# Optimization experiments

Measured on AMD Instinct MI355X. Metric: run time of the kernel, lower is better.

## Reference

```python
import jax, jax.numpy as jnp
import numpy as np

N, M, KNN, KUP, POS_DIM = 15872, 35637, 5, 20, 32


def _pos_emb_table(n, d):
    # transformer-style sinusoidal table (matches PosEmb._define_pos_emb)
    pos = np.arange(n, dtype=np.float32)[:, None]
    i2 = np.arange(0, d, 2, dtype=np.float32)
    div = 10000.0 ** (i2 / d)
    pe = np.zeros((n, d), dtype=np.float32)
    pe[:, 0::2] = np.sin(pos / div)
    pe[:, 1::2] = np.cos(pos / div)
    return jnp.asarray(pe)


def _lrelu(x):
    return jnp.where(x > 0, x, 0.2 * x)


def _gather(x, idx):
    # x: [B,n,d], idx: [B,m,k] -> [B,m,k,d]
    return jax.vmap(lambda xb, ib: xb[ib])(x, idx)


def _knn_idx(x, k):
    # x: [B,n,d]; k nearest excluding self (torch knn drops column 0 of topk)
    xx = jnp.sum(x * x, axis=-1)
    neg = 2.0 * jnp.einsum('bnd,bmd->bnm', x, x) - xx[:, :, None] - xx[:, None, :]
    _, idx = jax.lax.top_k(neg, k + 1)
    return idx[..., 1:]


def _emb_block(feat, idx, ec_w1, ec_s1, ec_h1, ec_w2, ec_b2,
               w1, s1, h1, w2, s2, h2, w3, s3, h3, w4, b4):
    # get_graph_feature: [B,n,k,2*in] = cat(nbr - ctr, ctr)
    nbr = _gather(feat, idx)
    ctr = jnp.broadcast_to(feat[:, :, None, :], nbr.shape)
    e = jnp.concatenate([nbr - ctr, ctr], axis=-1)
    # edge_conv (1x1 conv2d = per-edge linear); BN folded into scale/shift (eval mode)
    e = _lrelu(jnp.einsum('bnkc,oc->bnko', e, ec_w1) * ec_s1 + ec_h1)
    e = jnp.einsum('bnkc,oc->bnko', e, ec_w2) + ec_b2
    f1 = jnp.max(e, axis=2)                                   # max over k neighbors -> [B,n,out]
    fmax = jnp.broadcast_to(jnp.max(f1, axis=1, keepdims=True), f1.shape)
    favg = jnp.broadcast_to(jnp.mean(f1, axis=1, keepdims=True), f1.shape)
    h = jnp.concatenate([feat, f1, fmax, favg], axis=-1)      # [B,n,3*out+in]
    # fc_out: 1x1 conv1d stack = per-point MLP with folded BN + LeakyReLU
    h = _lrelu(h @ w1.T * s1 + h1)
    h = _lrelu(h @ w2.T * s2 + h2)
    h = _lrelu(h @ w3.T * s3 + h3)
    return h @ w4.T + b4


def _forward(lx, ldx, pos_emb,
             b0_ec_w1, b0_ec_s1, b0_ec_h1, b0_ec_w2, b0_ec_b2,
             b0_fc_w1, b0_fc_s1, b0_fc_h1, b0_fc_w2, b0_fc_s2, b0_fc_h2,
             b0_fc_w3, b0_fc_s3, b0_fc_h3, b0_fc_w4, b0_fc_b4,
             b1_ec_w1, b1_ec_s1, b1_ec_h1, b1_ec_w2, b1_ec_b2,
             b1_fc_w1, b1_fc_s1, b1_fc_h1, b1_fc_w2, b1_fc_s2, b1_fc_h2,
             b1_fc_w3, b1_fc_s3, b1_fc_h3, b1_fc_w4, b1_fc_b4,
             up_inputs, up_w0, up_s0, up_h0, up_w_rest, up_s_rest, up_h_rest, up_wf, up_bf,
             dec_w0, dec_b0, dec_w1, dec_b1, dec_w2, dec_b2, dec_w3, dec_b3,
             dec_w4, dec_b4, dec_wf, dec_bf,
             idx0, up_idx):
    B = ldx.shape[0]
    feat_in = jnp.concatenate([ldx, jnp.broadcast_to(pos_emb[None], (B,) + pos_emb.shape)], axis=-1)  # [B,N,35]
    f0 = _emb_block(feat_in, idx0,
                    b0_ec_w1, b0_ec_s1, b0_ec_h1, b0_ec_w2, b0_ec_b2,
                    b0_fc_w1, b0_fc_s1, b0_fc_h1, b0_fc_w2, b0_fc_s2, b0_fc_h2,
                    b0_fc_w3, b0_fc_s3, b0_fc_h3, b0_fc_w4, b0_fc_b4)   # [B,N,64]
    idx1 = _knn_idx(f0, KNN)                                            # dynamic feature-space KNN
    f1 = _emb_block(f0, idx1,
                    b1_ec_w1, b1_ec_s1, b1_ec_h1, b1_ec_w2, b1_ec_b2,
                    b1_fc_w1, b1_fc_s1, b1_fc_h1, b1_fc_w2, b1_fc_s2, b1_fc_h2,
                    b1_fc_w3, b1_fc_s3, b1_fc_h3, b1_fc_w4, b1_fc_b4)   # [B,N,128]
    x_feat = jnp.concatenate([feat_in, f0, f1], axis=-1)                # [B,N,227]
    # Upscale: SIREN-activated 1x1-conv stack -> softmax interpolation weights over KUP lo-res nbrs
    h = jnp.sin(jnp.einsum('bmkc,oc->bmko', up_inputs[:B], up_w0) * up_s0 + up_h0)
    for i in range(up_w_rest.shape[0]):
        h = jnp.sin(jnp.einsum('bmkc,oc->bmko', h, up_w_rest[i]) * up_s_rest[i] + up_h_rest[i])
    logits = jnp.einsum('bmkc,oc->bmko', h, up_wf) + up_bf              # [B,M,KUP,1]
    w = jax.nn.softmax(logits, axis=2)
    grouped = _gather(x_feat, up_idx)                                   # [B,M,KUP,227]
    z = jnp.sum(w * grouped, axis=2)                                    # [B,M,227]
    # SIREN decoder: dims [227,256,128,64,32,16,3]; zip with 5 mods applies first 5 layers + head
    h = jnp.sin(30.0 * (z @ dec_w0.T + dec_b0))
    h = jnp.sin(h @ dec_w1.T + dec_b1)
    h = jnp.sin(h @ dec_w2.T + dec_b2)
    h = jnp.sin(h @ dec_w3.T + dec_b3)
    h = jnp.sin(h @ dec_w4.T + dec_b4)
    return h @ dec_wf.T + dec_bf                                        # [B,M,3]


def setup_inputs():
    key = jax.random.key(0)
    ks = iter(jax.random.split(key, 100))
    def rn(*s):
        return jax.random.normal(next(ks), s, jnp.float32) * 0.05
    def sc(*s):
        return jax.random.uniform(next(ks), s, jnp.float32, minval=0.5, maxval=1.5)
    inp = {}
    inp['lx'] = jax.random.normal(next(ks), (1, N, 3), jnp.float32)
    inp['ldx'] = jax.random.normal(next(ks), (1, N, 3), jnp.float32)
    inp['pos_emb'] = _pos_emb_table(N, POS_DIM)
    inp['idx0'] = jax.random.randint(next(ks), (1, N, KNN), 0, N - 1)
    # EmbModule 0: in=35, out=64
    inp['b0_ec_w1'], inp['b0_ec_s1'], inp['b0_ec_h1'] = rn(128, 70), sc(128), rn(128)
    inp['b0_ec_w2'], inp['b0_ec_b2'] = rn(64, 128), rn(64)
    inp['b0_fc_w1'], inp['b0_fc_s1'], inp['b0_fc_h1'] = rn(192, 227), sc(192), rn(192)
    inp['b0_fc_w2'], inp['b0_fc_s2'], inp['b0_fc_h2'] = rn(128, 192), sc(128), rn(128)
    inp['b0_fc_w3'], inp['b0_fc_s3'], inp['b0_fc_h3'] = rn(64, 128), sc(64), rn(64)
    inp['b0_fc_w4'], inp['b0_fc_b4'] = rn(64, 64), rn(64)
    # EmbModule 1: in=64, out=128
    inp['b1_ec_w1'], inp['b1_ec_s1'], inp['b1_ec_h1'] = rn(256, 128), sc(256), rn(256)
    inp['b1_ec_w2'], inp['b1_ec_b2'] = rn(128, 256), rn(128)
    inp['b1_fc_w1'], inp['b1_fc_s1'], inp['b1_fc_h1'] = rn(384, 448), sc(384), rn(384)
    inp['b1_fc_w2'], inp['b1_fc_s2'], inp['b1_fc_h2'] = rn(256, 384), sc(256), rn(256)
    inp['b1_fc_w3'], inp['b1_fc_s3'], inp['b1_fc_h3'] = rn(128, 256), sc(128), rn(128)
    inp['b1_fc_w4'], inp['b1_fc_b4'] = rn(128, 128), rn(128)
    inp['up_inputs'] = jax.random.uniform(next(ks), (1, M, KUP, 7), jnp.float32)
    inp['up_idx'] = jax.random.randint(next(ks), (1, M, KUP), 0, N - 1)
    inp['up_w0'], inp['up_s0'], inp['up_h0'] = rn(128, 7), sc(128), rn(128)
    inp['up_w_rest'], inp['up_s_rest'], inp['up_h_rest'] = rn(7, 128, 128), sc(7, 128), rn(7, 128)
    inp['up_wf'], inp['up_bf'] = rn(1, 128), rn(1)
    # SIREN decoder
    dd = [227, 256, 128, 64, 32, 16]
    for i in range(5):
        inp['dec_w%d' % i], inp['dec_b%d' % i] = rn(dd[i + 1], dd[i]), rn(dd[i + 1])
    inp['dec_wf'], inp['dec_bf'] = rn(3, 16), rn(3)
    return inp


def reference(lx, ldx, pos_emb, idx0,
              b0_ec_w1, b0_ec_s1, b0_ec_h1, b0_ec_w2, b0_ec_b2,
              b0_fc_w1, b0_fc_s1, b0_fc_h1, b0_fc_w2, b0_fc_s2, b0_fc_h2,
              b0_fc_w3, b0_fc_s3, b0_fc_h3, b0_fc_w4, b0_fc_b4,
              b1_ec_w1, b1_ec_s1, b1_ec_h1, b1_ec_w2, b1_ec_b2,
              b1_fc_w1, b1_fc_s1, b1_fc_h1, b1_fc_w2, b1_fc_s2, b1_fc_h2,
              b1_fc_w3, b1_fc_s3, b1_fc_h3, b1_fc_w4, b1_fc_b4,
              up_inputs, up_idx, up_w0, up_s0, up_h0,
              up_w_rest, up_s_rest, up_h_rest, up_wf, up_bf,
              dec_w0, dec_b0, dec_w1, dec_b1, dec_w2, dec_b2, dec_w3, dec_b3,
              dec_w4, dec_b4, dec_wf, dec_bf):
    return _forward(lx, ldx, pos_emb,
                    b0_ec_w1, b0_ec_s1, b0_ec_h1, b0_ec_w2, b0_ec_b2,
                    b0_fc_w1, b0_fc_s1, b0_fc_h1, b0_fc_w2, b0_fc_s2, b0_fc_h2,
                    b0_fc_w3, b0_fc_s3, b0_fc_h3, b0_fc_w4, b0_fc_b4,
                    b1_ec_w1, b1_ec_s1, b1_ec_h1, b1_ec_w2, b1_ec_b2,
                    b1_fc_w1, b1_fc_s1, b1_fc_h1, b1_fc_w2, b1_fc_s2, b1_fc_h2,
                    b1_fc_w3, b1_fc_s3, b1_fc_h3, b1_fc_w4, b1_fc_b4,
                    up_inputs, up_w0, up_s0, up_h0, up_w_rest, up_s_rest, up_h_rest, up_wf, up_bf,
                    dec_w0, dec_b0, dec_w1, dec_b1, dec_w2, dec_b2, dec_w3, dec_b3,
                    dec_w4, dec_b4, dec_wf, dec_bf,
                    idx0, up_idx)
```

## Files before the change

### kernel.cpp

```cpp
#include <hip/hip_runtime.h>
#include <hip/hip_bf16.h>
#include <math.h>

#define N_PTS 15872
#define M_PTS 35637
#define KNN_K 5
#define KUP   20
#define UP_ROWS (M_PTS * KUP)
#define NTILE (N_PTS/32)
#define N_EDGE (N_PTS*KNN_K)
#define CDIV(a,b) (((a)+(b)-1)/(b))

typedef __hip_bfloat16 bf16;
typedef unsigned int uint;
typedef unsigned short ushort_t;
__device__ __forceinline__ float b2f(bf16 x){ return __bfloat162float(x); }

__device__ __forceinline__ uint f2bf_bits(float x){
  uint u = __float_as_uint(x);
  return (u + 0x7FFFu + ((u>>16)&1u)) >> 16;
}

__device__ __forceinline__ ushort_t f2h_bits(float x){
  union { _Float16 h; ushort_t u; } c; c.h = (_Float16)x; return c.u;
}

typedef __attribute__((ext_vector_type(8))) short bf16x8;
typedef __attribute__((ext_vector_type(8))) _Float16 f16x8;
typedef __attribute__((ext_vector_type(2))) __fp16 fp16x2_t;
typedef __attribute__((ext_vector_type(16))) float f32x16;
union FragAB { bf16x8 v; uint u[4]; };
union FragB  { bf16x8 v; uint4 q; };
union FragH  { f16x8 v; uint4 q; _Float16 h[8]; };
union Acc16  { f32x16 v; float f[16]; };
union H2U    { fp16x2_t h; uint u; };

__global__ void flag_k(const uint* __restrict__ pos_raw, int* __restrict__ flag){
  if (threadIdx.x == 0 && blockIdx.x == 0)
    flag[0] = (pos_raw[0] == 0x3F800000u) ? 1 : 0;
}

struct CvtTab { const void* src[52]; int start[52]; };
__global__ __launch_bounds__(256) void cvt_all_k(CvtTab tab, float* __restrict__ dst,
                                                 const int* __restrict__ flag, int total){
  int i = blockIdx.x*256 + threadIdx.x;
  if (i >= total) return;
  int s = 0;
#pragma unroll 1
  for (int k = 1; k < 52; k++) if (tab.start[k] <= i) s = k;
  int off = i - tab.start[s];
  float v = flag[0] ? b2f(((const bf16*)tab.src[s])[off]) : ((const float*)tab.src[s])[off];
  dst[i] = v;
}

__global__ void packfrag16_k(const float* __restrict__ w, const float* __restrict__ sr,
                             ushort_t* __restrict__ out, int n){
  int i = blockIdx.x*256 + threadIdx.x;
  if (i >= n) return;
  int j = i & 7;
  int lam = (i >> 3) & 63;
  int fg = i >> 9;
  int t = fg & 3, ks = (fg >> 2) & 1, Q = (fg >> 3) & 3, l = fg >> 5;
  int nn = t*32 + (lam & 31);
  int kk = Q*32 + ks*16 + (lam >> 5)*8 + j;
  float x = w[l*16384 + nn*128 + kk] * sr[l*128 + nn];
  out[i] = f2h_bits(x);
}

__global__ void packw_mfma_k(const float* __restrict__ w, ushort_t* __restrict__ whi,
                             ushort_t* __restrict__ wlo, int N, int K, int Kpad, int total){
  int i = blockIdx.x*256 + threadIdx.x;
  if (i >= total) return;
  int j = i & 7;
  int lane = (i >> 3) & 63;
  int fr = i >> 9;
  int nq = Kpad >> 5;
  int ks = fr & 1;
  int q  = (fr >> 1) % nq;
  int nt = (fr >> 1) / nq;
  int n = nt*32 + (lane & 31);
  int k = q*32 + ks*16 + (lane >> 5)*8 + j;
  float x = (n < N && k < K) ? w[(size_t)n*K + k] : 0.f;
  uint hb = f2bf_bits(x);
  uint lb = f2bf_bits(x - __uint_as_float(hb << 16));
  whi[i] = (ushort_t)hb;
  wlo[i] = (ushort_t)lb;
}

__global__ void packknn_k(const float* __restrict__ xf, const float* __restrict__ nr,
                          ushort_t* __restrict__ ahi, ushort_t* __restrict__ alo,
                          ushort_t* __restrict__ bhi, ushort_t* __restrict__ blo){
  int i = blockIdx.x*256 + threadIdx.x;
  if (i >= NTILE*5*64*8) return;
  int e = i & 7;
  int lane = (i >> 3) & 63;
  int rest = i >> 9;
  int kc = rest % 5, jt = rest / 5;
  int n = jt*32 + (lane & 31);
  int k = kc*16 + (lane >> 5)*8 + e;
  float f = (k < 64) ? xf[(size_t)n*227 + 35 + k] : 0.f;
  float av, bv;
  if (k < 64)      { av = 2.f*f;   bv = f; }
  else if (k == 64){ av = nr[n];   bv = -1.f; }
  else if (k == 65){ av = 1.f;     bv = -nr[n]; }
  else             { av = 0.f;     bv = 0.f; }
  uint ah = f2bf_bits(av); uint al = f2bf_bits(av - __uint_as_float(ah<<16));
  uint bh = f2bf_bits(bv); uint bl = f2bf_bits(bv - __uint_as_float(bh<<16));
  ahi[i] = (ushort_t)ah; alo[i] = (ushort_t)al;
  bhi[i] = (ushort_t)bh; blo[i] = (ushort_t)bl;
}

__global__ void fillmark_k(bf16* __restrict__ out, int n){
  int i = blockIdx.x*256 + threadIdx.x;
  if (i < n) out[i] = __float2bfloat16(12345.0f);
}

template<int EPI, int ACT>
__global__ __launch_bounds__(256) void gemm_k(
    const float* __restrict__ A, int lda,
    const float* __restrict__ W, int ldw,
    const float* __restrict__ scale, const float* __restrict__ shift,
    float gmul, float* __restrict__ C, int ldc,
    int M, int Nout, int K)
{
  __shared__ __align__(16) float As[16][64];
  __shared__ __align__(16) float Ws[16][64];
  const int tid = threadIdx.x;
  const int tx = tid & 15, ty = tid >> 4;
  const int bm = blockIdx.x * 64, bn = blockIdx.y * 64;
  const int ar = tid >> 2, ak = (tid & 3) * 4;
  float acc[4][4] = {};
  for (int k0 = 0; k0 < K; k0 += 16) {
    float a0=0.f,a1=0.f,a2=0.f,a3=0.f;
    int grow = bm + ar;
    if (grow < M) {
      const float* ap = A + (size_t)grow * lda + (k0 + ak);
      int rem = K - (k0 + ak);
      if (rem >= 4) { a0=ap[0]; a1=ap[1]; a2=ap[2]; a3=ap[3]; }
      else { if(rem>0)a0=ap[0]; if(rem>1)a1=ap[1]; if(rem>2)a2=ap[2]; }
    }
    float w0=0.f,w1=0.f,w2=0.f,w3=0.f;
    int gn = bn + ar;
    if (gn < Nout) {
      const float* wp = W + (size_t)gn * ldw + (k0 + ak);
      int rem = K - (k0 + ak);
      if (rem >= 4) { w0=wp[0]; w1=wp[1]; w2=wp[2]; w3=wp[3]; }
      else { if(rem>0)w0=wp[0]; if(rem>1)w1=wp[1]; if(rem>2)w2=wp[2]; }
    }
    __syncthreads();
    As[ak+0][ar]=a0; As[ak+1][ar]=a1; As[ak+2][ar]=a2; As[ak+3][ar]=a3;
    Ws[ak+0][ar]=w0; Ws[ak+1][ar]=w1; Ws[ak+2][ar]=w2; Ws[ak+3][ar]=w3;
    __syncthreads();
#pragma unroll
    for (int kk = 0; kk < 16; kk++) {
      float4 av = *reinterpret_cast<const float4*>(&As[kk][ty*4]);
      float4 wv = *reinterpret_cast<const float4*>(&Ws[kk][tx*4]);
      float aa[4] = {av.x,av.y,av.z,av.w};
      float ww[4] = {wv.x,wv.y,wv.z,wv.w};
#pragma unroll
      for (int i=0;i<4;i++)
#pragma unroll
        for (int j=0;j<4;j++) acc[i][j] += aa[i]*ww[j];
    }
  }
#pragma unroll
  for (int i=0;i<4;i++){
    int m = bm + ty*4 + i;
    if (m >= M) continue;
#pragma unroll
    for (int j=0;j<4;j++){
      int n = bn + tx*4 + j;
      if (n >= Nout) continue;
      float v = acc[i][j];
      if (EPI==0)      v = v * scale[n] + shift[n];
      else if (EPI==1) v = v + shift[n];
      else             v = (v + shift[n]) * gmul;
      if (ACT==1)      v = v > 0.f ? v : 0.2f*v;
      else if (ACT==2) v = sinf(v);
      C[(size_t)m*ldc + n] = v;
    }
  }
}

struct MLayer { int K, N, Kq, Nt, woff, soff, hoff, epi, act; float gmul; };
struct MCfg { MLayer L[6]; };

template<int NL, int OUTMODE>
__global__ __launch_bounds__(256) void mlp_fused_k(
    const float* __restrict__ A0, int lda0, int K0, int M,
    MCfg cfg,
    const ushort_t* __restrict__ wh, const ushort_t* __restrict__ wl,
    const float* __restrict__ wc,
    float* __restrict__ Cout, int ldc,
    void* __restrict__ oflg, const int* __restrict__ flag)
{
  __shared__ __align__(16) uint slab[64*256];
  const int tid = threadIdx.x;
  const int lane = tid & 63;
  const int wv = tid >> 6;
  const int np = lane & 31;
  const int hb2 = lane >> 5;
  const int rhalf = wv & 1, thalf = wv >> 1;
  const int rb = blockIdx.x * 64;
  const int row_l = rhalf*32 + np;

  for (int e = tid; e < 64*64; e += 256) {
    int r = e >> 6, g = e & 63;
    int gr = rb + r;
    uint p[4];
#pragma unroll
    for (int u=0;u<4;u++){
      int k = g*4+u;
      float f = (gr < M && k < K0) ? A0[(size_t)gr*lda0 + k] : 0.f;
      uint hb = f2bf_bits(f);
      uint lb = f2bf_bits(f - __uint_as_float(hb<<16));
      p[u] = (hb<<16) | lb;
    }
    *(uint4*)&slab[r*256 + (((g ^ r) & 63)<<2)] = make_uint4(p[0],p[1],p[2],p[3]);
  }
  __syncthreads();

#pragma unroll 1
  for (int l = 0; l < NL; l++){
    const int N = cfg.L[l].N, Kq = cfg.L[l].Kq, Nt = cfg.L[l].Nt;
    const int woff = cfg.L[l].woff, soff = cfg.L[l].soff, hoff = cfg.L[l].hoff;
    const int epi = cfg.L[l].epi, actf = cfg.L[l].act;
    const float gmul = cfg.L[l].gmul;
    Acc16 acc[4];
#pragma unroll
    for (int u=0;u<4;u++)
#pragma unroll
      for (int i=0;i<16;i++) acc[u].f[i] = 0.f;

#pragma unroll 1
    for (int q = 0; q < Kq; q++){
#pragma unroll
      for (int ks = 0; ks < 2; ks++){
        int g0 = (q*32 + ks*16 + hb2*8) >> 2;
        uint4 a0 = *(const uint4*)&slab[row_l*256 + ((((g0  ) ^ row_l) & 63)<<2)];
        uint4 a1 = *(const uint4*)&slab[row_l*256 + ((((g0+1) ^ row_l) & 63)<<2)];
        uint au[8] = {a0.x,a0.y,a0.z,a0.w,a1.x,a1.y,a1.z,a1.w};
        FragAB ah, al;
#pragma unroll
        for (int p=0;p<4;p++){
          ah.u[p] = (au[2*p]>>16)     | (au[2*p+1] & 0xFFFF0000u);
          al.u[p] = (au[2*p]&0xFFFFu) | (au[2*p+1]<<16);
        }
#pragma unroll
        for (int u=0;u<4;u++){
          int t = thalf + u*2;
          if (t < Nt){
            size_t fb = (size_t)woff + ((size_t)((t*Kq + q)*2 + ks))*512 + (size_t)lane*8;
            FragB bh, bl;
            bh.q = *(const uint4*)(wh + fb);
            bl.q = *(const uint4*)(wl + fb);
            acc[u].v = __builtin_amdgcn_mfma_f32_32x32x16_bf16(ah.v, bh.v, acc[u].v, 0,0,0);
            acc[u].v = __builtin_amdgcn_mfma_f32_32x32x16_bf16(al.v, bh.v, acc[u].v, 0,0,0);
            acc[u].v = __builtin_amdgcn_mfma_f32_32x32x16_bf16(ah.v, bl.v, acc[u].v, 0,0,0);
          }
        }
      }
    }
    __syncthreads();
#pragma unroll
    for (int u=0;u<4;u++){
      int t = thalf + u*2;
      if (t < Nt){
        int col = t*32 + np;
        if (col < N){
          float scv = (epi==0) ? wc[soff+col] : 0.f;
          float shv = wc[hoff+col];
#pragma unroll
          for (int reg=0;reg<16;reg++){
            int r32 = (reg&3) + 8*(reg>>2) + 4*hb2;
            float v = acc[u].f[reg];
            if (epi==0)      v = v*scv + shv;
            else if (epi==1) v = v + shv;
            else             v = (v + shv)*gmul;
            if (actf==1)      v = v > 0.f ? v : 0.2f*v;
            else if (actf==2) v = __sinf(v);
            if (l == NL-1){
              int gr = rb + rhalf*32 + r32;
              if (gr < M){
                if (OUTMODE==0) Cout[(size_t)gr*ldc + col] = v;
                else {
                  if (!(fabsf(v) < 1e30f)) v = 777.0f;
                  size_t oi = (size_t)gr*3 + col;
                  if (flag[0]) ((bf16*)oflg)[oi] = __float2bfloat16(v);
                  else         ((float*)oflg)[oi] = v;
                }
              }
            } else {
              int r = rhalf*32 + r32;
              uint hb = f2bf_bits(v);
              uint lb = f2bf_bits(v - __uint_as_float(hb<<16));
              slab[r*256 + ((((col>>2) ^ r) & 63)<<2) + (col&3)] = (hb<<16) | lb;
            }
          }
        }
      }
    }
    __syncthreads();
  }
}

#define INS5(tv, tj, v, j) \
  if ((v) > tv[4]){ tv[4]=(v); tj[4]=(j); \
    _Pragma("unroll") \
    for (int q=4;q>0;q--) \
      if (tv[q] > tv[q-1]){ float tf=tv[q-1]; tv[q-1]=tv[q]; tv[q]=tf; \
                            int ti=tj[q-1]; tj[q-1]=tj[q]; tj[q]=ti; } }

__global__ __launch_bounds__(256) void knn_mfma_k(
    const ushort_t* __restrict__ ahi, const ushort_t* __restrict__ alo,
    const ushort_t* __restrict__ bhi, const ushort_t* __restrict__ blo,
    int* __restrict__ out)
{
  __shared__ float mv[4][32][5];
  __shared__ int   mjj[4][32][5];
  const int tid = threadIdx.x;
  const int lane = tid & 63;
  const int wv = tid >> 6;
  const int np = lane & 31;
  const int hb2 = lane >> 5;
  const int it = blockIdx.x;
  const int ig = it*32 + np;

  FragB vh[5], vl[5];
  {
    size_t bb = (size_t)(it*5)*512 + (size_t)lane*8;
#pragma unroll
    for (int kc=0;kc<5;kc++){
      vh[kc].q = *(const uint4*)(bhi + bb + kc*512);
      vl[kc].q = *(const uint4*)(blo + bb + kc*512);
    }
  }

  float tv[5] = {-1e30f,-1e30f,-1e30f,-1e30f,-1e30f};
  int   tj[5] = {0,0,0,0,0};

  FragB uh[5], ul[5], nh[5], nl[5];
  {
    size_t ab = (size_t)(wv*5)*512 + (size_t)lane*8;
#pragma unroll
    for (int kc=0;kc<5;kc++){
      uh[kc].q = *(const uint4*)(ahi + ab + kc*512);
      ul[kc].q = *(const uint4*)(alo + ab + kc*512);
    }
  }

#pragma unroll 1
  for (int t = 0; t < NTILE/4; t++){
    int jt = wv + t*4;
    if (t+1 < NTILE/4){
      size_t an = (size_t)((jt+4)*5)*512 + (size_t)lane*8;
#pragma unroll
      for (int kc=0;kc<5;kc++){
        nh[kc].q = *(const uint4*)(ahi + an + kc*512);
        nl[kc].q = *(const uint4*)(alo + an + kc*512);
      }
    }
    Acc16 acc;
#pragma unroll
    for (int q=0;q<16;q++) acc.f[q] = 0.f;
#pragma unroll
    for (int kc=0;kc<5;kc++){
      acc.v = __builtin_amdgcn_mfma_f32_32x32x16_bf16(uh[kc].v, vh[kc].v, acc.v, 0,0,0);
      acc.v = __builtin_amdgcn_mfma_f32_32x32x16_bf16(ul[kc].v, vh[kc].v, acc.v, 0,0,0);
      acc.v = __builtin_amdgcn_mfma_f32_32x32x16_bf16(uh[kc].v, vl[kc].v, acc.v, 0,0,0);
    }
    int jb = jt*32 + 4*hb2;
#pragma unroll
    for (int reg=0;reg<16;reg++){
      int j = jb + (reg&3) + 8*(reg>>2);
      float v = acc.f[reg];
      if (j != ig) { INS5(tv, tj, v, j); }
    }
    if (t+1 < NTILE/4){
#pragma unroll
      for (int kc=0;kc<5;kc++){ uh[kc] = nh[kc]; ul[kc] = nl[kc]; }
    }
  }

#pragma unroll
  for (int s=0;s<5;s++){
    float ov = __shfl_xor(tv[s], 32, 64);
    int   oj = __shfl_xor(tj[s], 32, 64);
    INS5(tv, tj, ov, oj);
  }
  if (hb2 == 0){
#pragma unroll
    for (int s=0;s<5;s++){ mv[wv][np][s] = tv[s]; mjj[wv][np][s] = tj[s]; }
  }
  __syncthreads();
  if (tid < 32){
    float bv[5]; int bj[5];
#pragma unroll
    for (int s=0;s<5;s++){ bv[s] = mv[0][tid][s]; bj[s] = mjj[0][tid][s]; }
#pragma unroll
    for (int w=1;w<4;w++)
#pragma unroll
      for (int s=0;s<5;s++){
        float v = mv[w][tid][s]; int j = mjj[w][tid][s];
        INS5(bv, bj, v, j);
      }
    int gi = it*32 + tid;
#pragma unroll
    for (int s=0;s<5;s++) out[gi*KNN_K + s] = bj[s];
  }
}

__global__ __launch_bounds__(256) void siren_fused_k(
    const void* __restrict__ upin,
    const ushort_t* __restrict__ wf16,
    const float* __restrict__ W0c, const float* __restrict__ S0c, const float* __restrict__ H0c,
    const float* __restrict__ HRc,
    const float* __restrict__ WFc, const float* __restrict__ BFc,
    float* __restrict__ logits, const int* __restrict__ flag)
{
  __shared__ __align__(16) ushort_t act[4*32*128];
  __shared__ float intile[4*32*8];
  __shared__ __align__(16) float w0s[128*8];
  __shared__ __align__(16) float hrs[7*128];
  __shared__ float wfs[128];
  __shared__ float bfs[1];

  const int tid  = threadIdx.x;
  const int lane = tid & 63;
  const int wv   = tid >> 6;
  const int np   = lane & 31;
  const int hb2  = lane >> 5;
  const int npx  = np & 15;
  const int rowbase = blockIdx.x * 128 + wv * 32;
  const int isbf = flag[0];
  ushort_t* actw = act + wv*32*128;
  float* intw = intile + wv*32*8;
  const int abase = np*128;

  for (int e = tid; e < 128*7; e += 256){
    int c = e/7, k = e%7;
    w0s[c*8+k] = W0c[e]*S0c[c];
  }
  if (tid < 128) w0s[tid*8+7] = H0c[tid];
  for (int e = tid; e < 7*128; e += 256) hrs[e] = HRc[e];
  if (tid < 128) wfs[tid] = WFc[tid];
  if (tid == 0) bfs[0] = BFc[0];
  for (int e = lane; e < 32*7; e += 64) {
    int r = e/7, k = e%7;
    int gr = rowbase + r;
    float v = 0.f;
    if (gr < UP_ROWS)
      v = isbf ? b2f(((const bf16*)upin)[(size_t)gr*7+k]) : ((const float*)upin)[(size_t)gr*7+k];
    intw[r*8+k] = v;
  }
  __syncthreads();

  {
    float xin[7];
#pragma unroll
    for (int k=0;k<7;k++) xin[k] = intw[np*8+k];
#pragma unroll
    for (int gg = 0; gg < 8; gg++) {
      int g = hb2*8 + gg;
      float x[8];
#pragma unroll
      for (int j=0;j<8;j++){
        int c = g*8 + j;
        const float4 wa = *(const float4*)&w0s[c*8];
        const float4 wb = *(const float4*)&w0s[c*8+4];
        float a = wb.w;
        a += xin[0]*wa.x; a += xin[1]*wa.y; a += xin[2]*wa.z; a += xin[3]*wa.w;
        a += xin[4]*wb.x; a += xin[5]*wb.y; a += xin[6]*wb.z;
        x[j] = __sinf(a);
      }
      H2U c0,c1,c2,c3;
      c0.h = __builtin_amdgcn_cvt_pkrtz(x[0],x[1]);
      c1.h = __builtin_amdgcn_cvt_pkrtz(x[2],x[3]);
      c2.h = __builtin_amdgcn_cvt_pkrtz(x[4],x[5]);
      c3.h = __builtin_amdgcn_cvt_pkrtz(x[6],x[7]);
      *(uint4*)&actw[abase + ((g ^ npx)<<3)] = make_uint4(c0.u,c1.u,c2.u,c3.u);
    }
  }

#pragma unroll 1
  for (int l = 0; l < 7; l++) {
    Acc16 acc[4];
#pragma unroll
    for (int t=0;t<4;t++)
#pragma unroll
      for (int i=0;i<16;i++) acc[t].f[i] = 0.f;

#pragma unroll 1
    for (int Q = 0; Q < 4; Q++) {
#pragma unroll
      for (int ks = 0; ks < 2; ks++) {
        int g = Q*4 + ks*2 + hb2;
        FragH af;
        af.q = *(const uint4*)&actw[abase + ((g ^ npx) << 3)];
        int fb = (((l*4 + Q)*2 + ks)*4 << 9) + lane*8;
#pragma unroll
        for (int t=0;t<4;t++){
          FragH bh;
          bh.q = *(const uint4*)(wf16 + fb + t*512);
          acc[t].v = __builtin_amdgcn_mfma_f32_32x32x16_f16(bh.v, af.v, acc[t].v, 0,0,0);
        }
      }
    }
#pragma unroll
    for (int t=0;t<4;t++){
#pragma unroll
      for (int rg=0;rg<4;rg++){
        int g = t*4 + rg;
        const float4 bb = *(const float4*)&hrs[l*128 + g*8 + 4*hb2];
        float x0 = __sinf(acc[t].f[rg*4+0] + bb.x);
        float x1 = __sinf(acc[t].f[rg*4+1] + bb.y);
        float x2 = __sinf(acc[t].f[rg*4+2] + bb.z);
        float x3 = __sinf(acc[t].f[rg*4+3] + bb.w);
        H2U u0,u1;
        u0.h = __builtin_amdgcn_cvt_pkrtz(x0,x1);
        u1.h = __builtin_amdgcn_cvt_pkrtz(x2,x3);
        *(uint2*)&actw[abase + ((g ^ npx)<<3) + 4*hb2] = make_uint2(u0.u,u1.u);
      }
    }
  }

  {
    float a = 0.f;
#pragma unroll
    for (int g = 0; g < 8; g++) {
      int gg = hb2*8 + g;
      FragH u;
      u.q = *(const uint4*)&actw[abase + ((gg ^ npx) << 3)];
      int kb = gg*8;
#pragma unroll
      for (int e = 0; e < 8; e++) a += (float)u.h[e] * wfs[kb+e];
    }
    a += __shfl_xor(a, 32, 64);
    int gr = rowbase + np;
    if (hb2 == 0 && gr < UP_ROWS) logits[gr] = a + bfs[0];
  }
}

__global__ void featin_k(const void* __restrict__ ldx, const void* __restrict__ pos,
                         float* __restrict__ xf, const int* __restrict__ flag){
  int i = blockIdx.x*256 + threadIdx.x;
  if (i >= N_PTS*35) return;
  int n = i / 35, c = i % 35;
  float v;
  if (flag[0]) {
    v = (c < 3) ? b2f(((const bf16*)ldx)[n*3+c]) : b2f(((const bf16*)pos)[n*32 + (c-3)]);
  } else {
    v = (c < 3) ? ((const float*)ldx)[n*3+c] : ((const float*)pos)[n*32 + (c-3)];
  }
  xf[(size_t)n*227 + c] = v;
}

__global__ void gather_e_k(const float* __restrict__ xf, int coff, int CIN,
                           const int* __restrict__ idx, float* __restrict__ e,
                           int n0, int np){
  int W2 = 2*CIN;
  int i = blockIdx.x*256 + threadIdx.x;
  if (i >= np*KNN_K*W2) return;
  int c = i % W2; int ek = i / W2;
  int nl = ek / KNN_K, k = ek % KNN_K;
  int n = n0 + nl;
  int j = idx[n*KNN_K + k];
  float out;
  if (c < CIN) out = xf[(size_t)j*227 + coff + c] - xf[(size_t)n*227 + coff + c];
  else         out = xf[(size_t)n*227 + coff + (c-CIN)];
  e[(size_t)ek*W2 + c] = out;
}

__global__ void kmax_k(const float* __restrict__ e2, int C, float* __restrict__ f1,
                       int n0, int np){
  int i = blockIdx.x*256 + threadIdx.x;
  if (i >= np*C) return;
  int nl = i / C, c = i % C;
  float v = -1e30f;
  for (int k=0;k<KNN_K;k++) v = fmaxf(v, e2[((size_t)nl*KNN_K+k)*C + c]);
  f1[(size_t)(n0+nl)*C + c] = v;
}

template<int C>
__global__ __launch_bounds__(256) void reduce1_k(const float* __restrict__ X, int n,
                                                 float* __restrict__ pmax, float* __restrict__ psum){
  const int tid = threadIdx.x;
  const int c = tid % C;
  const int r0 = tid / C;
  const int TPR = 256 / C;
  float vmax = -1e30f, vsum = 0.f;
  for (int row = blockIdx.x * TPR + r0; row < n; row += gridDim.x * TPR) {
    float v = X[(size_t)row * C + c];
    vmax = fmaxf(vmax, v); vsum += v;
  }
  __shared__ float smax[256], ssum[256];
  smax[tid]=vmax; ssum[tid]=vsum;
  __syncthreads();
  if (tid < C) {
    for (int q=1;q<TPR;q++){ vmax=fmaxf(vmax, smax[q*C+c]); vsum += ssum[q*C+c]; }
    pmax[blockIdx.x*C + c] = vmax; psum[blockIdx.x*C + c] = vsum;
  }
}

template<int C>
__global__ void reduce2_k(const float* __restrict__ pmax, const float* __restrict__ psum,
                          int nblk, float invn, float* __restrict__ fmaxo, float* __restrict__ favgo){
  int c = threadIdx.x; if (c >= C) return;
  float vmax=-1e30f, vsum=0.f;
  for (int b=0;b<nblk;b++){ vmax=fmaxf(vmax,pmax[b*C+c]); vsum+=psum[b*C+c]; }
  fmaxo[c]=vmax; favgo[c]=vsum*invn;
}

__global__ void concat_k(const float* __restrict__ xf, int coff, int CF,
                         const float* __restrict__ f1, int C,
                         const float* __restrict__ fmax, const float* __restrict__ favg,
                         float* __restrict__ h, int n0, int np){
  int W = CF + 3*C;
  int i = blockIdx.x*256 + threadIdx.x;
  if (i >= np*W) return;
  int nl = i / W, c = i % W;
  int n = n0 + nl;
  float v;
  if (c < CF)          v = xf[(size_t)n*227 + coff + c];
  else if (c < CF+C)   v = f1[(size_t)n*C + (c-CF)];
  else if (c < CF+2*C) v = fmax[c-CF-C];
  else                 v = favg[c-CF-2*C];
  h[(size_t)nl*W + c] = v;
}

__global__ void norms_k(const float* __restrict__ xf, float* __restrict__ nr){
  int n = blockIdx.x*256 + threadIdx.x;
  if (n >= N_PTS) return;
  const float* p = xf + (size_t)n*227 + 35;
  float s = 0.f;
  for (int d=0;d<64;d++) s += p[d]*p[d];
  nr[n] = s;
}

__global__ __launch_bounds__(64) void softgather_k(const float* __restrict__ logits,
                                                   const int* __restrict__ up_idx,
                                                   const float* __restrict__ xf,
                                                   float* __restrict__ z){
  __shared__ float lw[KUP]; __shared__ int li[KUP];
  int m = blockIdx.x;
  int tid = threadIdx.x;
  if (tid < KUP){ lw[tid] = logits[(size_t)m*KUP + tid]; li[tid] = up_idx[(size_t)m*KUP + tid]; }
  __syncthreads();
  float mx = -1e30f;
  for (int k=0;k<KUP;k++) mx = fmaxf(mx, lw[k]);
  __syncthreads();
  if (tid < KUP) lw[tid] = expf(lw[tid]-mx);
  __syncthreads();
  float s = 0.f;
  for (int k=0;k<KUP;k++) s += lw[k];
  float inv = 1.f/s;
  for (int c = tid; c < 227; c += 64){
    float acc = 0.f;
    for (int k=0;k<KUP;k++) acc += lw[k] * xf[(size_t)li[k]*227 + c];
    z[(size_t)m*227 + c] = acc*inv;
  }
}

extern "C" void kernel_launch(void* const* d_in, const int* in_sizes, int n_in,
                              void* d_out, int out_size, void* d_ws, size_t ws_size,
                              hipStream_t stream) {
  const int *idx0  = (const int*)d_in[3];
  const int *upidx = (const int*)d_in[37];

  float* ws = (float*)d_ws;
  float* x_feat = ws;
  float* f1b    = ws + 3602944;
  float* pmax   = ws + 5634560;
  float* psum   = ws + 5667328;
  float* fmaxv  = ws + 5700096;
  float* favgv  = ws + 5700224;
  int*   flag   = (int*)(ws + 5700352);
  int*   idx1   = (int*)(ws + 5700368);
  float* nrm    = ws + 5779728;
  float* logits = ws + 5795600;
  float* wcvt   = ws + 6508352;
  float* S      = ws + 7214400;
  ushort_t* whi  = (ushort_t*)(S + 9662464);
  ushort_t* wlo  = whi + 114688;
  ushort_t* gwhi = wlo + 114688;
  ushort_t* gwlo = gwhi + 331776;

  const size_t NEED = (size_t)(7214400 + 9662464) * 4
                    + (size_t)(114688*2 + 331776*2) * 2;
  if (ws_size < NEED) {
    fillmark_k<<<CDIV(out_size,256),256,0,stream>>>((bf16*)d_out, out_size);
    return;
  }

  flag_k<<<1,64,0,stream>>>((const uint*)d_in[2], flag);
  CvtTab tab;
  int wcoff = 0, seg = 0;
  auto CVT = [&](int i, int n)->const float* {
    tab.src[seg] = d_in[i]; tab.start[seg] = wcoff; seg++;
    const float* p = wcvt + wcoff; wcoff += n;
    return p;
  };
  const float *E0W1=CVT(4,8960),  *E0S1=CVT(5,128),  *E0H1=CVT(6,128),
              *E0W2=CVT(7,8192),  *E0B2=CVT(8,64);
  const float *F0W1=CVT(9,43584), *F0S1=CVT(10,192), *F0H1=CVT(11,192),
              *F0W2=CVT(12,24576),*F0S2=CVT(13,128), *F0H2=CVT(14,128),
              *F0W3=CVT(15,8192), *F0S3=CVT(16,64),  *F0H3=CVT(17,64),
              *F0W4=CVT(18,4096), *F0B4=CVT(19,64);
  const float *E1W1=CVT(20,32768),*E1S1=CVT(21,256), *E1H1=CVT(22,256),
              *E1W2=CVT(23,32768),*E1B2=CVT(24,128);
  const float *F1W1=CVT(25,172032),*F1S1=CVT(26,384),*F1H1=CVT(27,384),
              *F1W2=CVT(28,98304),*F1S2=CVT(29,256), *F1H2=CVT(30,256),
              *F1W3=CVT(31,32768),*F1S3=CVT(32,128), *F1H3=CVT(33,128),
              *F1W4=CVT(34,16384),*F1B4=CVT(35,128);
  const float *UPW0=CVT(38,896),  *UPS0=CVT(39,128), *UPH0=CVT(40,128),
              *UPWR=CVT(41,114688),*UPSR=CVT(42,896),*UPHR=CVT(43,896),
              *UPWF=CVT(44,128),  *UPBF=CVT(45,1);
  const float *DW0=CVT(46,58112), *DB0=CVT(47,256),
              *DW1=CVT(48,32768), *DB1=CVT(49,128),
              *DW2=CVT(50,8192),  *DB2=CVT(51,64),
              *DW3=CVT(52,2048),  *DB3=CVT(53,32),
              *DW4=CVT(54,512),   *DB4=CVT(55,16),
              *DWF=CVT(56,48),    *DBF=CVT(57,3);
  cvt_all_k<<<CDIV(wcoff,256),256,0,stream>>>(tab, wcvt, flag, wcoff);

  packfrag16_k<<<CDIV(114688,256),256,0,stream>>>(UPWR, UPSR, whi, 114688);

  int offs[16]; const float* srcs[16]; int Ns[16], Ks[16], Kps[16];
  {
    int o = 0, q = 0;
    auto REG = [&](const float* s, int N, int K, int Kpad){
      srcs[q]=s; Ns[q]=N; Ks[q]=K; Kps[q]=Kpad; offs[q]=o;
      o += CDIV(N,32)*32*Kpad; q++;
    };
    REG(F0W1,192,227,256); REG(F0W2,128,192,192); REG(F0W3,64,128,128); REG(F0W4,64,64,64);
    REG(DW0,256,227,256);  REG(DW1,128,256,256);  REG(DW2,64,128,128);
    REG(DW3,32,64,64);     REG(DW4,16,32,32);     REG(DWF,3,16,32);
    REG(E0W1,128,70,96);   REG(E0W2,64,128,128);
    REG(E1W1,256,128,128); REG(E1W2,128,256,256);
    REG(F1W3,128,256,256); REG(F1W4,128,128,128);
  }
  for (int q = 0; q < 16; q++){
    int total = CDIV(Ns[q],32)*32*Kps[q];
    packw_mfma_k<<<CDIV(total,256),256,0,stream>>>(srcs[q], gwhi+offs[q], gwlo+offs[q],
                                                   Ns[q], Ks[q], Kps[q], total);
  }

  auto OFF = [&](const float* p){ return (int)(p - wcvt); };
  MCfg cfc0{};
  cfc0.L[0] = {227,192,8,6, offs[0], OFF(F0S1), OFF(F0H1), 0,1, 0.f};
  cfc0.L[1] = {192,128,6,4, offs[1], OFF(F0S2), OFF(F0H2), 0,1, 0.f};
  cfc0.L[2] = {128, 64,4,2, offs[2], OFF(F0S3), OFF(F0H3), 0,1, 0.f};
  cfc0.L[3] = { 64, 64,2,2, offs[3], 0,         OFF(F0B4), 1,0, 0.f};
  MCfg cdec{};
  cdec.L[0] = {227,256,8,8, offs[4], 0, OFF(DB0), 2,2, 30.f};
  cdec.L[1] = {256,128,8,4, offs[5], 0, OFF(DB1), 1,2, 0.f};
  cdec.L[2] = {128, 64,4,2, offs[6], 0, OFF(DB2), 1,2, 0.f};
  cdec.L[3] = { 64, 32,2,1, offs[7], 0, OFF(DB3), 1,2, 0.f};
  cdec.L[4] = { 32, 16,1,1, offs[8], 0, OFF(DB4), 1,2, 0.f};
  cdec.L[5] = { 16,  3,1,1, offs[9], 0, OFF(DBF), 1,0, 0.f};
  MCfg ce0{};
  ce0.L[0] = { 70,128,3,4, offs[10], OFF(E0S1), OFF(E0H1), 0,1, 0.f};
  ce0.L[1] = {128, 64,4,2, offs[11], 0,         OFF(E0B2), 1,0, 0.f};
  MCfg ce1{};
  ce1.L[0] = {128,256,4,8, offs[12], OFF(E1S1), OFF(E1H1), 0,1, 0.f};
  ce1.L[1] = {256,128,8,4, offs[13], 0,         OFF(E1B2), 1,0, 0.f};
  MCfg cf1t{};
  cf1t.L[0] = {256,128,8,4, offs[14], OFF(F1S3), OFF(F1H3), 0,1, 0.f};
  cf1t.L[1] = {128,128,4,4, offs[15], 0,         OFF(F1B4), 1,0, 0.f};

  const float invN = 1.f/(float)N_PTS;
  const int CHN = 8192;

  featin_k<<<CDIV(N_PTS*35,256),256,0,stream>>>(d_in[1], d_in[2], x_feat, flag);

  {
    const int P0 = N_PTS/2;
    for (int n0 = 0; n0 < N_PTS; n0 += P0) {
      int ne = P0 * KNN_K;
      float* eA   = S;
      float* eOut = S + 2777600;
      gather_e_k<<<CDIV(ne*70,256),256,0,stream>>>(x_feat, 0, 35, idx0, eA, n0, P0);
      mlp_fused_k<2,0><<<CDIV(ne,64),256,0,stream>>>(
          eA,70,70,ne, ce0, gwhi,gwlo,wcvt, eOut,64, nullptr, flag);
      kmax_k<<<CDIV(P0*64,256),256,0,stream>>>(eOut, 64, f1b, n0, P0);
    }
  }
  reduce1_k<64><<<256,256,0,stream>>>(f1b, N_PTS, pmax, psum);
  reduce2_k<64><<<1,64,0,stream>>>(pmax, psum, 256, invN, fmaxv, favgv);
  {
    float* h = S;
    concat_k<<<CDIV(N_PTS*227,256),256,0,stream>>>(x_feat,0,35, f1b,64, fmaxv,favgv, h, 0, N_PTS);
    mlp_fused_k<4,0><<<CDIV(N_PTS,64),256,0,stream>>>(
        h,227,227,N_PTS, cfc0, gwhi,gwlo,wcvt, x_feat+35,227, nullptr, flag);
  }

  norms_k<<<CDIV(N_PTS,256),256,0,stream>>>(x_feat, nrm);
  {
    const int PLANE = NTILE*5*64*8;
    ushort_t* ajhi = (ushort_t*)S;
    ushort_t* ajlo = ajhi + PLANE;
    ushort_t* bihi = ajlo + PLANE;
    ushort_t* bilo = bihi + PLANE;
    packknn_k<<<CDIV(PLANE,256),256,0,stream>>>(x_feat, nrm, ajhi, ajlo, bihi, bilo);
    knn_mfma_k<<<NTILE,256,0,stream>>>(ajhi, ajlo, bihi, bilo, idx1);
  }

  {
    const int P1 = 5952;
    for (int n0 = 0; n0 < N_PTS; n0 += P1) {
      int np = N_PTS - n0; if (np > P1) np = P1;
      int ne = np * KNN_K;
      float* eA   = S;
      float* eOut = S + 3809280;
      gather_e_k<<<CDIV(ne*128,256),256,0,stream>>>(x_feat, 35, 64, idx1, eA, n0, np);
      mlp_fused_k<2,0><<<CDIV(ne,64),256,0,stream>>>(
          eA,128,128,ne, ce1, gwhi,gwlo,wcvt, eOut,128, nullptr, flag);
      kmax_k<<<CDIV(np*128,256),256,0,stream>>>(eOut, 128, f1b, n0, np);
    }
  }
  reduce1_k<128><<<256,256,0,stream>>>(f1b, N_PTS, pmax, psum);
  reduce2_k<128><<<1,128,0,stream>>>(pmax, psum, 256, invN, fmaxv, favgv);
  for (int n0 = 0; n0 < N_PTS; n0 += CHN) {
    int np = N_PTS - n0; if (np > CHN) np = CHN;
    float* h  = S;
    float* a1 = S + 3670016;
    int gx = CDIV(np,64);
    concat_k<<<CDIV(np*448,256),256,0,stream>>>(x_feat,35,64, f1b,128, fmaxv,favgv, h, n0, np);
    gemm_k<0,1><<<dim3(gx,6),256,0,stream>>>(h,448,  F1W1,448, F1S1,F1H1,0.f, a1,384, np,384,448);
    gemm_k<0,1><<<dim3(gx,4),256,0,stream>>>(a1,384, F1W2,384, F1S2,F1H2,0.f, h,256,  np,256,384);
    mlp_fused_k<2,0><<<gx,256,0,stream>>>(
        h,256,256,np, cf1t, gwhi,gwlo,wcvt, x_feat+(size_t)n0*227+99,227, nullptr, flag);
  }

  siren_fused_k<<<CDIV(UP_ROWS,128),256,0,stream>>>(
      d_in[36], whi, UPW0, UPS0, UPH0, UPHR, UPWF, UPBF, logits, flag);
  float* zbuf = S;
  softgather_k<<<M_PTS,64,0,stream>>>(logits, upidx, x_feat, zbuf);

  mlp_fused_k<6,1><<<CDIV(M_PTS,64),256,0,stream>>>(
      zbuf,227,227,M_PTS, cdec, gwhi,gwlo,wcvt, nullptr,0, d_out, flag);
}
```

Baseline: 2.052 ms.

## Keep SIREN layer activations in registers via lane shuffles instead of LDS

The fused SIREN MLP kernel no longer writes each layer's fp16 activations to a swizzled shared-memory tile and reads them back as MFMA operands. It holds the MFMA output fragments in registers and builds the next layer's input fragments with cross-half-wave shuffles (PSWAP). The MFMA loop is also restructured to process two output tiles at a time across all 8 K-steps. This removes LDS traffic and the 32KB activation buffer, but adds register pressure and shuffle instructions.

```diff
diff --git a/kernel.cpp b/kernel.cpp
--- a/kernel.cpp
+++ b/kernel.cpp
@@ -34,6 +34,13 @@
 union FragH  { f16x8 v; uint4 q; _Float16 h[8]; };
 union Acc16  { f32x16 v; float f[16]; };
 union H2U    { fp16x2_t h; uint u; };
+
+#define PSWAP(a,b) { \
+  unsigned _ax = (unsigned)__shfl_xor((int)(a), 32, 64); \
+  unsigned _bx = (unsigned)__shfl_xor((int)(b), 32, 64); \
+  unsigned _na = hb2 ? _bx : (a); \
+  unsigned _nb = hb2 ? (b) : _ax; \
+  (a) = _na; (b) = _nb; }
 
 __global__ void flag_k(const uint* __restrict__ pos_raw, int* __restrict__ flag){
   if (threadIdx.x == 0 && blockIdx.x == 0)
@@ -418,11 +425,10 @@
     const float* __restrict__ WFc, const float* __restrict__ BFc,
     float* __restrict__ logits, const int* __restrict__ flag)
 {
-  __shared__ __align__(16) ushort_t act[4*32*128];
   __shared__ float intile[4*32*8];
   __shared__ __align__(16) float w0s[128*8];
   __shared__ __align__(16) float hrs[7*128];
-  __shared__ float wfs[128];
+  __shared__ __align__(16) float wfs[128];
   __shared__ float bfs[1];
 
   const int tid  = threadIdx.x;
@@ -430,12 +436,9 @@
   const int wv   = tid >> 6;
   const int np   = lane & 31;
   const int hb2  = lane >> 5;
-  const int npx  = np & 15;
   const int rowbase = blockIdx.x * 128 + wv * 32;
   const int isbf = flag[0];
-  ushort_t* actw = act + wv*32*128;
   float* intw = intile + wv*32*8;
-  const int abase = np*128;
 
   for (int e = tid; e < 128*7; e += 256){
     int c = e/7, k = e%7;
@@ -455,71 +458,89 @@
   }
   __syncthreads();
 
+  uint st0[16], st1[16];
   {
     float xin[7];
 #pragma unroll
     for (int k=0;k<7;k++) xin[k] = intw[np*8+k];
 #pragma unroll
-    for (int gg = 0; gg < 8; gg++) {
-      int g = hb2*8 + gg;
-      float x[8];
-#pragma unroll
-      for (int j=0;j<8;j++){
-        int c = g*8 + j;
+    for (int g = 0; g < 16; g++){
+      float xs[4];
+#pragma unroll
+      for (int j = 0; j < 4; j++){
+        int c = g*8 + hb2*4 + j;
         const float4 wa = *(const float4*)&w0s[c*8];
         const float4 wb = *(const float4*)&w0s[c*8+4];
         float a = wb.w;
         a += xin[0]*wa.x; a += xin[1]*wa.y; a += xin[2]*wa.z; a += xin[3]*wa.w;
         a += xin[4]*wb.x; a += xin[5]*wb.y; a += xin[6]*wb.z;
-        x[j] = __sinf(a);
+        xs[j] = __sinf(a);
       }
-      H2U c0,c1,c2,c3;
-      c0.h = __builtin_amdgcn_cvt_pkrtz(x[0],x[1]);
-      c1.h = __builtin_amdgcn_cvt_pkrtz(x[2],x[3]);
-      c2.h = __builtin_amdgcn_cvt_pkrtz(x[4],x[5]);
-      c3.h = __builtin_amdgcn_cvt_pkrtz(x[6],x[7]);
-      *(uint4*)&actw[abase + ((g ^ npx)<<3)] = make_uint4(c0.u,c1.u,c2.u,c3.u);
-    }
-  }
-
+      H2U u0,u1;
+      u0.h = __builtin_amdgcn_cvt_pkrtz(xs[0],xs[1]);
+      u1.h = __builtin_amdgcn_cvt_pkrtz(xs[2],xs[3]);
+      st0[g] = u0.u; st1[g] = u1.u;
+    }
+  }
+
+  FragH fr[8];
+#pragma unroll
+  for (int m = 0; m < 8; m++){
+    uint a0 = st0[2*m], b0 = st0[2*m+1];
+    uint a1 = st1[2*m], b1 = st1[2*m+1];
+    PSWAP(a0,b0); PSWAP(a1,b1);
+    fr[m].q = make_uint4(a0, a1, b0, b1);
+  }
+
+  uint nst0[16], nst1[16];
 #pragma unroll 1
   for (int l = 0; l < 7; l++) {
-    Acc16 acc[4];
-#pragma unroll
-    for (int t=0;t<4;t++)
-#pragma unroll
-      for (int i=0;i<16;i++) acc[t].f[i] = 0.f;
-
-#pragma unroll 1
-    for (int Q = 0; Q < 4; Q++) {
-#pragma unroll
-      for (int ks = 0; ks < 2; ks++) {
-        int g = Q*4 + ks*2 + hb2;
-        FragH af;
-        af.q = *(const uint4*)&actw[abase + ((g ^ npx) << 3)];
-        int fb = (((l*4 + Q)*2 + ks)*4 << 9) + lane*8;
-#pragma unroll
-        for (int t=0;t<4;t++){
-          FragH bh;
-          bh.q = *(const uint4*)(wf16 + fb + t*512);
-          acc[t].v = __builtin_amdgcn_mfma_f32_32x32x16_f16(bh.v, af.v, acc[t].v, 0,0,0);
-        }
+#pragma unroll
+    for (int tp = 0; tp < 2; tp++){
+      Acc16 acc0, acc1;
+#pragma unroll
+      for (int i=0;i<16;i++){ acc0.f[i] = 0.f; acc1.f[i] = 0.f; }
+#pragma unroll
+      for (int m = 0; m < 8; m++){
+        int fb = (((l*8 + m)*4 + tp*2) << 9) + lane*8;
+        FragH bh0, bh1;
+        bh0.q = *(const uint4*)(wf16 + fb);
+        bh1.q = *(const uint4*)(wf16 + fb + 512);
+        acc0.v = __builtin_amdgcn_mfma_f32_32x32x16_f16(bh0.v, fr[m].v, acc0.v, 0,0,0);
+        acc1.v = __builtin_amdgcn_mfma_f32_32x32x16_f16(bh1.v, fr[m].v, acc1.v, 0,0,0);
       }
-    }
-#pragma unroll
-    for (int t=0;t<4;t++){
-#pragma unroll
-      for (int rg=0;rg<4;rg++){
-        int g = t*4 + rg;
-        const float4 bb = *(const float4*)&hrs[l*128 + g*8 + 4*hb2];
-        float x0 = __sinf(acc[t].f[rg*4+0] + bb.x);
-        float x1 = __sinf(acc[t].f[rg*4+1] + bb.y);
-        float x2 = __sinf(acc[t].f[rg*4+2] + bb.z);
-        float x3 = __sinf(acc[t].f[rg*4+3] + bb.w);
+#pragma unroll
+      for (int rg = 0; rg < 4; rg++){
+        int g0 = (tp*2+0)*4 + rg;
+        const float4 b0v = *(const float4*)&hrs[l*128 + g0*8 + hb2*4];
+        float x0 = __sinf(acc0.f[rg*4+0] + b0v.x);
+        float x1 = __sinf(acc0.f[rg*4+1] + b0v.y);
+        float x2 = __sinf(acc0.f[rg*4+2] + b0v.z);
+        float x3 = __sinf(acc0.f[rg*4+3] + b0v.w);
         H2U u0,u1;
         u0.h = __builtin_amdgcn_cvt_pkrtz(x0,x1);
         u1.h = __builtin_amdgcn_cvt_pkrtz(x2,x3);
-        *(uint2*)&actw[abase + ((g ^ npx)<<3) + 4*hb2] = make_uint2(u0.u,u1.u);
+        nst0[g0] = u0.u; nst1[g0] = u1.u;
+
+        int g1 = (tp*2+1)*4 + rg;
+        const float4 b1v = *(const float4*)&hrs[l*128 + g1*8 + hb2*4];
+        float y0 = __sinf(acc1.f[rg*4+0] + b1v.x);
+        float y1 = __sinf(acc1.f[rg*4+1] + b1v.y);
+        float y2 = __sinf(acc1.f[rg*4+2] + b1v.z);
+        float y3 = __sinf(acc1.f[rg*4+3] + b1v.w);
+        H2U v0,v1;
+        v0.h = __builtin_amdgcn_cvt_pkrtz(y0,y1);
+        v1.h = __builtin_amdgcn_cvt_pkrtz(y2,y3);
+        nst0[g1] = v0.u; nst1[g1] = v1.u;
+      }
+    }
+    if (l < 6){
+#pragma unroll
+      for (int m = 0; m < 8; m++){
+        uint a0 = nst0[2*m], b0 = nst0[2*m+1];
+        uint a1 = nst1[2*m], b1 = nst1[2*m+1];
+        PSWAP(a0,b0); PSWAP(a1,b1);
+        fr[m].q = make_uint4(a0, a1, b0, b1);
       }
     }
   }
@@ -527,13 +548,11 @@
   {
     float a = 0.f;
 #pragma unroll
-    for (int g = 0; g < 8; g++) {
-      int gg = hb2*8 + g;
-      FragH u;
-      u.q = *(const uint4*)&actw[abase + ((gg ^ npx) << 3)];
-      int kb = gg*8;
-#pragma unroll
-      for (int e = 0; e < 8; e++) a += (float)u.h[e] * wfs[kb+e];
+    for (int g = 0; g < 16; g++){
+      const float4 w4 = *(const float4*)&wfs[g*8 + hb2*4];
+      H2U u0,u1; u0.u = nst0[g]; u1.u = nst1[g];
+      a += (float)u0.h.x*w4.x + (float)u0.h.y*w4.y
+         + (float)u1.h.x*w4.z + (float)u1.h.y*w4.w;
     }
     a += __shfl_xor(a, 32, 64);
     int gr = rowbase + np;
```

Result: faster. 1.994 ms (-2.8%).
